# Performance work log

Measured on AMD Instinct MI355X. Metric: run time of the kernel, lower is better.

## Reference

```python
import jax, jax.numpy as jnp
import numpy as np

N, M, D = 1024, 1024, 256


def setup_inputs() -> dict:
    key = jax.random.key(0)
    k1, k2 = jax.random.split(key)
    z_x = jax.random.normal(k1, (N, D), dtype=jnp.float32)
    z_y = jax.random.normal(k2, (M, D), dtype=jnp.float32)
    return {"z_x": z_x, "z_y": z_y}


def reference(z_x, z_y):
    # s[i, j] = -sum_d |z_x[i, d] - z_y[j, d]|   -> [N, M] negative L1 distances
    s = -jnp.sum(jnp.abs(z_x[:, None, :] - z_y[None, :, :]), axis=-1)
    a = jax.nn.softmax(s, axis=1)  # row-wise alignment probs
    b = jax.nn.softmax(s, axis=0)  # column-wise alignment probs
    w = a + b - a * b              # soft symmetric alignment weights
    # weighted mean similarity (scalar)
    c = jnp.sum(w * s) / jnp.sum(w)
    return c
```

## Files before the change

### kernel.cpp

```cpp
#include <hip/hip_runtime.h>
#include <math.h>

#define NN 1024
#define MM 1024
#define DD 256
#define TILE 64
#define NTB 16
#define PITCH 260

__device__ inline void merge_ms(float& m, float& s, float m2, float s2) {
  float mn = fmaxf(m, m2);
  s = s * __expf(m - mn) + s2 * __expf(m2 - mn);
  m = mn;
}

__device__ inline float wredSum(float v) {
#pragma unroll
  for (int o = 32; o > 0; o >>= 1) v += __shfl_down(v, o, 64);
  return v;
}

__global__ __launch_bounds__(256) void k_tile(const float* __restrict__ zx,
                                              const float* __restrict__ zy,
                                              float* __restrict__ S,
                                              float* __restrict__ rowPM,
                                              float* __restrict__ rowPS,
                                              float* __restrict__ colPM,
                                              float* __restrict__ colPS) {
  __shared__ float xs[TILE * PITCH];
  __shared__ float ys[TILE * PITCH];
  const int it = blockIdx.y, jt = blockIdx.x;
  const int i0 = it * TILE, j0 = jt * TILE;
  const int t = threadIdx.x;
  const int tx = t & 15, ty = t >> 4;

#pragma unroll
  for (int k = 0; k < 16; ++k) {
    int idx4 = t + k * 256;
    int r = idx4 >> 6;
    int c4 = idx4 & 63;
    float4 vx = reinterpret_cast<const float4*>(zx + (size_t)(i0 + r) * DD)[c4];
    float4 vy = reinterpret_cast<const float4*>(zy + (size_t)(j0 + r) * DD)[c4];
    *reinterpret_cast<float4*>(&xs[r * PITCH + c4 * 4]) = vx;
    *reinterpret_cast<float4*>(&ys[r * PITCH + c4 * 4]) = vy;
  }
  __syncthreads();

  float acc4[4][4] = {{0.f}};
  for (int d4 = 0; d4 < DD / 4; ++d4) {
    float4 xa[4], yb[4];
#pragma unroll
    for (int a = 0; a < 4; ++a)
      xa[a] = *reinterpret_cast<const float4*>(&xs[(ty + a * 16) * PITCH + d4 * 4]);
#pragma unroll
    for (int b = 0; b < 4; ++b)
      yb[b] = *reinterpret_cast<const float4*>(&ys[(tx + b * 16) * PITCH + d4 * 4]);
#pragma unroll
    for (int a = 0; a < 4; ++a)
#pragma unroll
      for (int b = 0; b < 4; ++b) {
        acc4[a][b] += fabsf(xa[a].x - yb[b].x) + fabsf(xa[a].y - yb[b].y) +
                      fabsf(xa[a].z - yb[b].z) + fabsf(xa[a].w - yb[b].w);
      }
  }

#pragma unroll
  for (int a = 0; a < 4; ++a) {
    int i = i0 + ty + a * 16;
#pragma unroll
    for (int b = 0; b < 4; ++b) {
      int j = j0 + tx + b * 16;
      S[(size_t)i * MM + j] = -acc4[a][b];
    }
  }

#pragma unroll
  for (int a = 0; a < 4; ++a) {
    float m = -acc4[a][0];
#pragma unroll
    for (int b = 1; b < 4; ++b) m = fmaxf(m, -acc4[a][b]);
    float s = 0.f;
#pragma unroll
    for (int b = 0; b < 4; ++b) s += __expf(-acc4[a][b] - m);
#pragma unroll
    for (int off = 1; off < 16; off <<= 1) {
      float m2 = __shfl_xor(m, off, 64);
      float s2 = __shfl_xor(s, off, 64);
      merge_ms(m, s, m2, s2);
    }
    if (tx == 0) {
      int i = i0 + ty + a * 16;
      rowPM[(size_t)jt * NN + i] = m;
      rowPS[(size_t)jt * NN + i] = s;
    }
  }

  __shared__ float lm[16][64];
  __shared__ float lsv[16][64];
#pragma unroll
  for (int b = 0; b < 4; ++b) {
    int c = tx + b * 16;
    float m = -acc4[0][b];
#pragma unroll
    for (int a = 1; a < 4; ++a) m = fmaxf(m, -acc4[a][b]);
    float s = 0.f;
#pragma unroll
    for (int a = 0; a < 4; ++a) s += __expf(-acc4[a][b] - m);
    lm[ty][c] = m;
    lsv[ty][c] = s;
  }
  __syncthreads();
  if (t < 64) {
    float m = lm[0][t], s = lsv[0][t];
#pragma unroll
    for (int k = 1; k < 16; ++k) merge_ms(m, s, lm[k][t], lsv[k][t]);
    colPM[(size_t)it * MM + j0 + t] = m;
    colPS[(size_t)it * MM + j0 + t] = s;
  }
}

__global__ __launch_bounds__(256) void k_merge(const float* __restrict__ rowPM,
                                               const float* __restrict__ rowPS,
                                               const float* __restrict__ colPM,
                                               const float* __restrict__ colPS,
                                               float* __restrict__ rowM,
                                               float* __restrict__ rowS,
                                               float* __restrict__ colM,
                                               float* __restrict__ colS) {
  int g = blockIdx.x * 256 + threadIdx.x;
  if (g < NN) {
    float m = rowPM[g], s = rowPS[g];
#pragma unroll
    for (int k = 1; k < NTB; ++k)
      merge_ms(m, s, rowPM[(size_t)k * NN + g], rowPS[(size_t)k * NN + g]);
    rowM[g] = m;
    rowS[g] = s;
  } else {
    int c = g - NN;
    float m = colPM[c], s = colPS[c];
#pragma unroll
    for (int k = 1; k < NTB; ++k)
      merge_ms(m, s, colPM[(size_t)k * MM + c], colPS[(size_t)k * MM + c]);
    colM[c] = m;
    colS[c] = s;
  }
}

__global__ __launch_bounds__(256) void k_accum(const float* __restrict__ S,
                                               const float* __restrict__ rowM,
                                               const float* __restrict__ rowS,
                                               const float* __restrict__ colM,
                                               const float* __restrict__ colS,
                                               float* __restrict__ bNum,
                                               float* __restrict__ bDen) {
  const int i = blockIdx.x;
  const int t = threadIdx.x;
  float4 v = reinterpret_cast<const float4*>(S + (size_t)i * MM)[t];
  const float rm = rowM[i];
  const float rinv = 1.f / rowS[i];
  float4 cm = reinterpret_cast<const float4*>(colM)[t];
  float4 cs = reinterpret_cast<const float4*>(colS)[t];
  float num = 0.f, den = 0.f;
#define DO_COMP(VX, CMX, CSX)               \
  {                                         \
    float a = __expf((VX) - rm) * rinv;     \
    float b = __expf((VX) - (CMX)) / (CSX); \
    float w = a + b - a * b;                \
    num += w * (VX);                        \
    den += w;                               \
  }
  DO_COMP(v.x, cm.x, cs.x)
  DO_COMP(v.y, cm.y, cs.y)
  DO_COMP(v.z, cm.z, cs.z)
  DO_COMP(v.w, cm.w, cs.w)
#undef DO_COMP
  num = wredSum(num);
  den = wredSum(den);
  __shared__ float rn[4], rd[4];
  const int lane = t & 63, wv = t >> 6;
  if (lane == 0) { rn[wv] = num; rd[wv] = den; }
  __syncthreads();
  if (t == 0) {
    bNum[i] = rn[0] + rn[1] + rn[2] + rn[3];
    bDen[i] = rd[0] + rd[1] + rd[2] + rd[3];
  }
}

__global__ __launch_bounds__(256) void k_final(const float* __restrict__ bNum,
                                               const float* __restrict__ bDen,
                                               float* __restrict__ out) {
  const int t = threadIdx.x;
  float4 n4 = reinterpret_cast<const float4*>(bNum)[t];
  float4 d4 = reinterpret_cast<const float4*>(bDen)[t];
  float n = n4.x + n4.y + n4.z + n4.w;
  float d = d4.x + d4.y + d4.z + d4.w;
  n = wredSum(n);
  d = wredSum(d);
  __shared__ float rn[4], rd[4];
  const int lane = t & 63, wv = t >> 6;
  if (lane == 0) { rn[wv] = n; rd[wv] = d; }
  __syncthreads();
  if (t == 0) out[0] = (rn[0] + rn[1] + rn[2] + rn[3]) / (rd[0] + rd[1] + rd[2] + rd[3]);
}

extern "C" void kernel_launch(void* const* d_in, const int* in_sizes, int n_in,
                              void* d_out, int out_size, void* d_ws, size_t ws_size,
                              hipStream_t stream) {
  const float* zx = (const float*)d_in[0];
  const float* zy = (const float*)d_in[1];
  float* out = (float*)d_out;

  float* ws = (float*)d_ws;
  float* S     = ws;
  float* rowPM = S + (size_t)NN * MM;
  float* rowPS = rowPM + NTB * NN;
  float* colPM = rowPS + NTB * NN;
  float* colPS = colPM + NTB * MM;
  float* rowM  = colPS + NTB * MM;
  float* rowS  = rowM + NN;
  float* colM  = rowS + NN;
  float* colS  = colM + MM;
  float* bNum  = colS + MM;
  float* bDen  = bNum + NN;

  k_tile<<<dim3(NTB, NTB), 256, 0, stream>>>(zx, zy, S, rowPM, rowPS, colPM, colPS);
  k_merge<<<8, 256, 0, stream>>>(rowPM, rowPS, colPM, colPS, rowM, rowS, colM, colS);
  k_accum<<<NN, 256, 0, stream>>>(S, rowM, rowS, colM, colS, bNum, bDen);
  k_final<<<1, 256, 0, stream>>>(bNum, bDen, out);
}
```

Baseline: 39.20 us.

## Fuse merge, accumulate and final reduction into one kernel with atomic last-block finish

Replaces the k_merge, k_accum and k_final kernels with a single k_wacc kernel. Each of its 64 blocks re-merges the column partial max/sum stats, merges the row stats for its own 16 rows, and accumulates the weights over those rows. The last block to finish, found through an atomic ticket counter that k_tile resets, performs the final reduction. The distance loop in k_tile is also rewritten with double-buffered register loads and split accumulation. This cuts two kernel launches, but every block now repeats the column merge, and only 64 blocks do the accumulation pass.

```diff
diff --git a/kernel.cpp b/kernel.cpp
--- a/kernel.cpp
+++ b/kernel.cpp
@@ -26,13 +26,16 @@
                                               float* __restrict__ rowPM,
                                               float* __restrict__ rowPS,
                                               float* __restrict__ colPM,
-                                              float* __restrict__ colPS) {
+                                              float* __restrict__ colPS,
+                                              int* __restrict__ counter) {
   __shared__ float xs[TILE * PITCH];
   __shared__ float ys[TILE * PITCH];
   const int it = blockIdx.y, jt = blockIdx.x;
   const int i0 = it * TILE, j0 = jt * TILE;
   const int t = threadIdx.x;
   const int tx = t & 15, ty = t >> 4;
+
+  if (it == 0 && jt == 0 && t == 0) counter[0] = 0;
 
 #pragma unroll
   for (int k = 0; k < 16; ++k) {
@@ -47,22 +50,36 @@
   __syncthreads();
 
   float acc4[4][4] = {{0.f}};
-  for (int d4 = 0; d4 < DD / 4; ++d4) {
-    float4 xa[4], yb[4];
-#pragma unroll
-    for (int a = 0; a < 4; ++a)
-      xa[a] = *reinterpret_cast<const float4*>(&xs[(ty + a * 16) * PITCH + d4 * 4]);
-#pragma unroll
-    for (int b = 0; b < 4; ++b)
-      yb[b] = *reinterpret_cast<const float4*>(&ys[(tx + b * 16) * PITCH + d4 * 4]);
-#pragma unroll
-    for (int a = 0; a < 4; ++a)
-#pragma unroll
-      for (int b = 0; b < 4; ++b) {
-        acc4[a][b] += fabsf(xa[a].x - yb[b].x) + fabsf(xa[a].y - yb[b].y) +
-                      fabsf(xa[a].z - yb[b].z) + fabsf(xa[a].w - yb[b].w);
-      }
-  }
+  float4 xa[4], yb[4], xa2[4], yb2[4];
+
+#define LOADF(XV, YV, D4)                                                        \
+  {                                                                              \
+    _Pragma("unroll") for (int a = 0; a < 4; ++a)                                \
+        XV[a] = *reinterpret_cast<const float4*>(&xs[(ty + a * 16) * PITCH + (D4) * 4]); \
+    _Pragma("unroll") for (int b = 0; b < 4; ++b)                                \
+        YV[b] = *reinterpret_cast<const float4*>(&ys[(tx + b * 16) * PITCH + (D4) * 4]); \
+  }
+
+#define COMPUTEF(XV, YV)                                        \
+  {                                                             \
+    _Pragma("unroll") for (int a = 0; a < 4; ++a)               \
+        _Pragma("unroll") for (int b = 0; b < 4; ++b) {         \
+      acc4[a][b] += fabsf(XV[a].x - YV[b].x);                   \
+      acc4[a][b] += fabsf(XV[a].y - YV[b].y);                   \
+      acc4[a][b] += fabsf(XV[a].z - YV[b].z);                   \
+      acc4[a][b] += fabsf(XV[a].w - YV[b].w);                   \
+    }                                                           \
+  }
+
+  LOADF(xa, yb, 0)
+  for (int d4 = 0; d4 < DD / 4; d4 += 2) {
+    LOADF(xa2, yb2, d4 + 1)
+    COMPUTEF(xa, yb)
+    if (d4 + 2 < DD / 4) LOADF(xa, yb, d4 + 2)
+    COMPUTEF(xa2, yb2)
+  }
+#undef LOADF
+#undef COMPUTEF
 
 #pragma unroll
   for (int a = 0; a < 4; ++a) {
@@ -119,61 +136,64 @@
   }
 }
 
-__global__ __launch_bounds__(256) void k_merge(const float* __restrict__ rowPM,
-                                               const float* __restrict__ rowPS,
-                                               const float* __restrict__ colPM,
-                                               const float* __restrict__ colPS,
-                                               float* __restrict__ rowM,
-                                               float* __restrict__ rowS,
-                                               float* __restrict__ colM,
-                                               float* __restrict__ colS) {
-  int g = blockIdx.x * 256 + threadIdx.x;
-  if (g < NN) {
-    float m = rowPM[g], s = rowPS[g];
+__global__ __launch_bounds__(256) void k_wacc(const float* __restrict__ S,
+                                              const float* __restrict__ rowPM,
+                                              const float* __restrict__ rowPS,
+                                              const float* __restrict__ colPM,
+                                              const float* __restrict__ colPS,
+                                              float* __restrict__ bNum,
+                                              float* __restrict__ bDen,
+                                              int* __restrict__ counter,
+                                              float* __restrict__ out) {
+  const int bid = blockIdx.x;
+  const int t = threadIdx.x;
+
+  float4 cm = reinterpret_cast<const float4*>(colPM)[t];
+  float4 cs = reinterpret_cast<const float4*>(colPS)[t];
+#pragma unroll
+  for (int k = 1; k < NTB; ++k) {
+    float4 m2 = reinterpret_cast<const float4*>(colPM + (size_t)k * MM)[t];
+    float4 s2 = reinterpret_cast<const float4*>(colPS + (size_t)k * MM)[t];
+    merge_ms(cm.x, cs.x, m2.x, s2.x);
+    merge_ms(cm.y, cs.y, m2.y, s2.y);
+    merge_ms(cm.z, cs.z, m2.z, s2.z);
+    merge_ms(cm.w, cs.w, m2.w, s2.w);
+  }
+  float4 ci;
+  ci.x = 1.f / cs.x; ci.y = 1.f / cs.y; ci.z = 1.f / cs.z; ci.w = 1.f / cs.w;
+
+  __shared__ float rowMl[16], rowIl[16];
+  if (t < 16) {
+    int r = bid * 16 + t;
+    float m = rowPM[r], s = rowPS[r];
 #pragma unroll
     for (int k = 1; k < NTB; ++k)
-      merge_ms(m, s, rowPM[(size_t)k * NN + g], rowPS[(size_t)k * NN + g]);
-    rowM[g] = m;
-    rowS[g] = s;
-  } else {
-    int c = g - NN;
-    float m = colPM[c], s = colPS[c];
-#pragma unroll
-    for (int k = 1; k < NTB; ++k)
-      merge_ms(m, s, colPM[(size_t)k * MM + c], colPS[(size_t)k * MM + c]);
-    colM[c] = m;
-    colS[c] = s;
-  }
-}
-
-__global__ __launch_bounds__(256) void k_accum(const float* __restrict__ S,
-                                               const float* __restrict__ rowM,
-                                               const float* __restrict__ rowS,
-                                               const float* __restrict__ colM,
-                                               const float* __restrict__ colS,
-                                               float* __restrict__ bNum,
-                                               float* __restrict__ bDen) {
-  const int i = blockIdx.x;
-  const int t = threadIdx.x;
-  float4 v = reinterpret_cast<const float4*>(S + (size_t)i * MM)[t];
-  const float rm = rowM[i];
-  const float rinv = 1.f / rowS[i];
-  float4 cm = reinterpret_cast<const float4*>(colM)[t];
-  float4 cs = reinterpret_cast<const float4*>(colS)[t];
+      merge_ms(m, s, rowPM[(size_t)k * NN + r], rowPS[(size_t)k * NN + r]);
+    rowMl[t] = m;
+    rowIl[t] = 1.f / s;
+  }
+  __syncthreads();
+
   float num = 0.f, den = 0.f;
-#define DO_COMP(VX, CMX, CSX)               \
-  {                                         \
-    float a = __expf((VX) - rm) * rinv;     \
-    float b = __expf((VX) - (CMX)) / (CSX); \
-    float w = a + b - a * b;                \
-    num += w * (VX);                        \
-    den += w;                               \
-  }
-  DO_COMP(v.x, cm.x, cs.x)
-  DO_COMP(v.y, cm.y, cs.y)
-  DO_COMP(v.z, cm.z, cs.z)
-  DO_COMP(v.w, cm.w, cs.w)
+  for (int rl = 0; rl < 16; ++rl) {
+    int row = bid * 16 + rl;
+    float4 v = reinterpret_cast<const float4*>(S + (size_t)row * MM)[t];
+    float rm = rowMl[rl], ri = rowIl[rl];
+#define DO_COMP(VX, CMX, CIX)               \
+    {                                       \
+      float a = __expf((VX) - rm) * ri;     \
+      float b = __expf((VX) - (CMX)) * (CIX); \
+      float w = a + b - a * b;              \
+      num += w * (VX);                      \
+      den += w;                             \
+    }
+    DO_COMP(v.x, cm.x, ci.x)
+    DO_COMP(v.y, cm.y, ci.y)
+    DO_COMP(v.z, cm.z, ci.z)
+    DO_COMP(v.w, cm.w, ci.w)
 #undef DO_COMP
+  }
+
   num = wredSum(num);
   den = wredSum(den);
   __shared__ float rn[4], rd[4];
@@ -181,26 +201,24 @@
   if (lane == 0) { rn[wv] = num; rd[wv] = den; }
   __syncthreads();
   if (t == 0) {
-    bNum[i] = rn[0] + rn[1] + rn[2] + rn[3];
-    bDen[i] = rd[0] + rd[1] + rd[2] + rd[3];
-  }
-}
-
-__global__ __launch_bounds__(256) void k_final(const float* __restrict__ bNum,
-                                               const float* __restrict__ bDen,
-                                               float* __restrict__ out) {
-  const int t = threadIdx.x;
-  float4 n4 = reinterpret_cast<const float4*>(bNum)[t];
-  float4 d4 = reinterpret_cast<const float4*>(bDen)[t];
-  float n = n4.x + n4.y + n4.z + n4.w;
-  float d = d4.x + d4.y + d4.z + d4.w;
-  n = wredSum(n);
-  d = wredSum(d);
-  __shared__ float rn[4], rd[4];
-  const int lane = t & 63, wv = t >> 6;
-  if (lane == 0) { rn[wv] = n; rd[wv] = d; }
-  __syncthreads();
-  if (t == 0) out[0] = (rn[0] + rn[1] + rn[2] + rn[3]) / (rd[0] + rd[1] + rd[2] + rd[3]);
+    bNum[bid] = rn[0] + rn[1] + rn[2] + rn[3];
+    bDen[bid] = rd[0] + rd[1] + rd[2] + rd[3];
+  }
+
+  __shared__ int isLast;
+  if (t == 0) {
+    __threadfence();
+    int ticket = atomicAdd(counter, 1);
+    isLast = (ticket == 63) ? 1 : 0;
+  }
+  __syncthreads();
+  if (isLast && t < 64) {
+    __threadfence();
+    float n = bNum[t], d = bDen[t];
+    n = wredSum(n);
+    d = wredSum(d);
+    if (t == 0) out[0] = n / d;
+  }
 }
 
 extern "C" void kernel_launch(void* const* d_in, const int* in_sizes, int n_in,
@@ -216,15 +234,10 @@
   float* rowPS = rowPM + NTB * NN;
   float* colPM = rowPS + NTB * NN;
   float* colPS = colPM + NTB * MM;
-  float* rowM  = colPS + NTB * MM;
-  float* rowS  = rowM + NN;
-  float* colM  = rowS + NN;
-  float* colS  = colM + MM;
-  float* bNum  = colS + MM;
-  float* bDen  = bNum + NN;
-
-  k_tile<<<dim3(NTB, NTB), 256, 0, stream>>>(zx, zy, S, rowPM, rowPS, colPM, colPS);
-  k_merge<<<8, 256, 0, stream>>>(rowPM, rowPS, colPM, colPS, rowM, rowS, colM, colS);
-  k_accum<<<NN, 256, 0, stream>>>(S, rowM, rowS, colM, colS, bNum, bDen);
-  k_final<<<1, 256, 0, stream>>>(bNum, bDen, out);
-}
+  float* bNum  = colPS + NTB * MM;
+  float* bDen  = bNum + 64;
+  int*   counter = (int*)(bDen + 64);
+
+  k_tile<<<dim3(NTB, NTB), 256, 0, stream>>>(zx, zy, S, rowPM, rowPS, colPM, colPS, counter);
+  k_wacc<<<64, 256, 0, stream>>>(S, rowPM, rowPS, colPM, colPS, bNum, bDen, counter, out);
+}
```

New measurement: 45.09 us. +15.0%, slower.

## Compute L1 distances in packed fp16 with fdot2 accumulation and smaller row tiles

Applied to the files above, without the earlier changes.

The tile kernel now converts z_x and z_y to fp16 when staging them in shared memory. Distances are computed with packed half subtraction, a bitmask absolute value and fdot2 accumulation into fp32, which cuts ALU instructions per element and halves LDS traffic. The row tile shrinks from 64 to 32, doubling the block count to improve CU occupancy, and the partial row/column merge buffers are resized to match. The cost is fp16 rounding of the inputs, and the softmax may amplify that error in the distances.

```diff
diff --git a/kernel.cpp b/kernel.cpp
--- a/kernel.cpp
+++ b/kernel.cpp
@@ -4,9 +4,28 @@
 #define NN 1024
 #define MM 1024
 #define DD 256
-#define TILE 64
-#define NTB 16
-#define PITCH 260
+#define TI 32
+#define TJ 64
+#define NTI 32
+#define NTJ 16
+#define PITCH_H 264
+
+typedef _Float16 f16x2 __attribute__((ext_vector_type(2)));
+typedef _Float16 f16x4 __attribute__((ext_vector_type(4)));
+
+__device__ inline f16x2 habs2(f16x2 v) {
+  unsigned u = __builtin_bit_cast(unsigned, v) & 0x7FFF7FFFu;
+  return __builtin_bit_cast(f16x2, u);
+}
+
+__device__ inline float dot2acc(f16x2 a, float acc) {
+#if __has_builtin(__builtin_amdgcn_fdot2)
+  const f16x2 one = {(_Float16)1.0f, (_Float16)1.0f};
+  return __builtin_amdgcn_fdot2(a, one, acc, false);
+#else
+  return acc + (float)a.x + (float)a.y;
+#endif
+}
 
 __device__ inline void merge_ms(float& m, float& s, float m2, float s2) {
   float mn = fmaxf(m, m2);
@@ -27,45 +46,60 @@
                                               float* __restrict__ rowPS,
                                               float* __restrict__ colPM,
                                               float* __restrict__ colPS) {
-  __shared__ float xs[TILE * PITCH];
-  __shared__ float ys[TILE * PITCH];
+  __shared__ __align__(16) _Float16 xs[TI * PITCH_H];
+  __shared__ __align__(16) _Float16 ys[TJ * PITCH_H];
+  __shared__ float lm[16][64];
+  __shared__ float lsv[16][64];
+
   const int it = blockIdx.y, jt = blockIdx.x;
-  const int i0 = it * TILE, j0 = jt * TILE;
+  const int i0 = it * TI, j0 = jt * TJ;
   const int t = threadIdx.x;
   const int tx = t & 15, ty = t >> 4;
 
+#pragma unroll
+  for (int k = 0; k < 8; ++k) {
+    int idx4 = t + k * 256;
+    int r = idx4 >> 6;
+    int c4 = idx4 & 63;
+    float4 v = reinterpret_cast<const float4*>(zx + (size_t)(i0 + r) * DD)[c4];
+    f16x4 h = {(_Float16)v.x, (_Float16)v.y, (_Float16)v.z, (_Float16)v.w};
+    *reinterpret_cast<f16x4*>(&xs[r * PITCH_H + c4 * 4]) = h;
+  }
 #pragma unroll
   for (int k = 0; k < 16; ++k) {
     int idx4 = t + k * 256;
     int r = idx4 >> 6;
     int c4 = idx4 & 63;
-    float4 vx = reinterpret_cast<const float4*>(zx + (size_t)(i0 + r) * DD)[c4];
-    float4 vy = reinterpret_cast<const float4*>(zy + (size_t)(j0 + r) * DD)[c4];
-    *reinterpret_cast<float4*>(&xs[r * PITCH + c4 * 4]) = vx;
-    *reinterpret_cast<float4*>(&ys[r * PITCH + c4 * 4]) = vy;
-  }
-  __syncthreads();
-
-  float acc4[4][4] = {{0.f}};
-  for (int d4 = 0; d4 < DD / 4; ++d4) {
-    float4 xa[4], yb[4];
-#pragma unroll
-    for (int a = 0; a < 4; ++a)
-      xa[a] = *reinterpret_cast<const float4*>(&xs[(ty + a * 16) * PITCH + d4 * 4]);
+    float4 v = reinterpret_cast<const float4*>(zy + (size_t)(j0 + r) * DD)[c4];
+    f16x4 h = {(_Float16)v.x, (_Float16)v.y, (_Float16)v.z, (_Float16)v.w};
+    *reinterpret_cast<f16x4*>(&ys[r * PITCH_H + c4 * 4]) = h;
+  }
+  __syncthreads();
+
+  float acc4[2][4] = {{0.f}};
+  for (int s8 = 0; s8 < 32; ++s8) {
+    uint4 xw[2], yw[4];
+#pragma unroll
+    for (int a = 0; a < 2; ++a)
+      xw[a] = *reinterpret_cast<const uint4*>(&xs[(ty + a * 16) * PITCH_H + s8 * 8]);
 #pragma unroll
     for (int b = 0; b < 4; ++b)
-      yb[b] = *reinterpret_cast<const float4*>(&ys[(tx + b * 16) * PITCH + d4 * 4]);
-#pragma unroll
-    for (int a = 0; a < 4; ++a)
+      yw[b] = *reinterpret_cast<const uint4*>(&ys[(tx + b * 16) * PITCH_H + s8 * 8]);
+#pragma unroll
+    for (int a = 0; a < 2; ++a)
 #pragma unroll
       for (int b = 0; b < 4; ++b) {
-        acc4[a][b] += fabsf(xa[a].x - yb[b].x) + fabsf(xa[a].y - yb[b].y) +
-                      fabsf(xa[a].z - yb[b].z) + fabsf(xa[a].w - yb[b].w);
+        float acc = acc4[a][b];
+        acc = dot2acc(habs2(__builtin_bit_cast(f16x2, xw[a].x) - __builtin_bit_cast(f16x2, yw[b].x)), acc);
+        acc = dot2acc(habs2(__builtin_bit_cast(f16x2, xw[a].y) - __builtin_bit_cast(f16x2, yw[b].y)), acc);
+        acc = dot2acc(habs2(__builtin_bit_cast(f16x2, xw[a].z) - __builtin_bit_cast(f16x2, yw[b].z)), acc);
+        acc = dot2acc(habs2(__builtin_bit_cast(f16x2, xw[a].w) - __builtin_bit_cast(f16x2, yw[b].w)), acc);
+        acc4[a][b] = acc;
       }
   }
 
 #pragma unroll
-  for (int a = 0; a < 4; ++a) {
+  for (int a = 0; a < 2; ++a) {
     int i = i0 + ty + a * 16;
 #pragma unroll
     for (int b = 0; b < 4; ++b) {
@@ -75,7 +109,7 @@
   }
 
 #pragma unroll
-  for (int a = 0; a < 4; ++a) {
+  for (int a = 0; a < 2; ++a) {
     float m = -acc4[a][0];
 #pragma unroll
     for (int b = 1; b < 4; ++b) m = fmaxf(m, -acc4[a][b]);
@@ -95,17 +129,11 @@
     }
   }
 
-  __shared__ float lm[16][64];
-  __shared__ float lsv[16][64];
 #pragma unroll
   for (int b = 0; b < 4; ++b) {
     int c = tx + b * 16;
-    float m = -acc4[0][b];
-#pragma unroll
-    for (int a = 1; a < 4; ++a) m = fmaxf(m, -acc4[a][b]);
-    float s = 0.f;
-#pragma unroll
-    for (int a = 0; a < 4; ++a) s += __expf(-acc4[a][b] - m);
+    float m = fmaxf(-acc4[0][b], -acc4[1][b]);
+    float s = __expf(-acc4[0][b] - m) + __expf(-acc4[1][b] - m);
     lm[ty][c] = m;
     lsv[ty][c] = s;
   }
@@ -131,7 +159,7 @@
   if (g < NN) {
     float m = rowPM[g], s = rowPS[g];
 #pragma unroll
-    for (int k = 1; k < NTB; ++k)
+    for (int k = 1; k < NTJ; ++k)
       merge_ms(m, s, rowPM[(size_t)k * NN + g], rowPS[(size_t)k * NN + g]);
     rowM[g] = m;
     rowS[g] = s;
@@ -139,7 +167,7 @@
     int c = g - NN;
     float m = colPM[c], s = colPS[c];
 #pragma unroll
-    for (int k = 1; k < NTB; ++k)
+    for (int k = 1; k < NTI; ++k)
       merge_ms(m, s, colPM[(size_t)k * MM + c], colPS[(size_t)k * MM + c]);
     colM[c] = m;
     colS[c] = s;
@@ -213,17 +241,17 @@
   float* ws = (float*)d_ws;
   float* S     = ws;
   float* rowPM = S + (size_t)NN * MM;
-  float* rowPS = rowPM + NTB * NN;
-  float* colPM = rowPS + NTB * NN;
-  float* colPS = colPM + NTB * MM;
-  float* rowM  = colPS + NTB * MM;
+  float* rowPS = rowPM + NTJ * NN;
+  float* colPM = rowPS + NTJ * NN;
+  float* colPS = colPM + NTI * MM;
+  float* rowM  = colPS + NTI * MM;
   float* rowS  = rowM + NN;
   float* colM  = rowS + NN;
   float* colS  = colM + MM;
   float* bNum  = colS + MM;
   float* bDen  = bNum + NN;
 
-  k_tile<<<dim3(NTB, NTB), 256, 0, stream>>>(zx, zy, S, rowPM, rowPS, colPM, colPS);
+  k_tile<<<dim3(NTJ, NTI), 256, 0, stream>>>(zx, zy, S, rowPM, rowPS, colPM, colPS);
   k_merge<<<8, 256, 0, stream>>>(rowPM, rowPS, colPM, colPS, rowM, rowS, colM, colS);
   k_accum<<<NN, 256, 0, stream>>>(S, rowM, rowS, colM, colS, bNum, bDen);
   k_final<<<1, 256, 0, stream>>>(bNum, bDen, out);
```

After: 32.30 us. -17.6%, faster.
